# Kernel optimization log

Hardware: AMD Instinct MI355X
Metric: run time of the kernel (lower is better)

The kernel has to match this reference:

```python
import jax, jax.numpy as jnp
import numpy as np

P = 8  # patch_shape (8, 8) -> per-window sequence length 64


def _bias_indices():
    # pairs of (i, j) coords inside an 8x8 patch window
    pairs = np.array([[i, j] for i in range(P) for j in range(P)])  # [64, 2]
    rel = pairs[:, None, :] - pairs[None, :, :] + P - 1  # [64, 64, 2] in [0, 14]
    return rel[:, :, 0], rel[:, :, 1]


def _make_mask(Wy, Wx):
    # generate_mask with apply_shift=True, patch_shape=(8,8)
    s = P // 2
    m = np.zeros((Wy, Wx, P, P, P, P), dtype=bool)
    m[-1, :, :s, :, s:, :] = True
    m[-1, :, s:, :, :s, :] = True
    m[:, -1, :, :s, :, s:] = True
    m[:, -1, :, s:, :, :s] = True
    return jnp.asarray(m.reshape(Wy, Wx, P * P, P * P))


def setup_inputs() -> dict:
    key = jax.random.key(0)
    ks = jax.random.split(key, 10)
    B, Wy, Wx, S, E, H, hd = 16, 16, 16, 64, 128, 4, 32
    sc = 0.05
    return {
        "patches": jax.random.normal(ks[0], (B, Wy, Wx, S, E), dtype=jnp.float32),
        "Wq": jax.random.normal(ks[1], (H, E, hd), dtype=jnp.float32) * sc,
        "bq": jax.random.normal(ks[2], (H, hd), dtype=jnp.float32) * sc,
        "Wk": jax.random.normal(ks[3], (H, E, hd), dtype=jnp.float32) * sc,
        "bk": jax.random.normal(ks[4], (H, hd), dtype=jnp.float32) * sc,
        "Wv": jax.random.normal(ks[5], (H, E, hd), dtype=jnp.float32) * sc,
        "bv": jax.random.normal(ks[6], (H, hd), dtype=jnp.float32) * sc,
        "pos_bias": jax.random.normal(ks[7], (2 * P - 1, 2 * P - 1), dtype=jnp.float32) * 0.02,
        "Wo": jax.random.normal(ks[8], (E, E), dtype=jnp.float32) * sc,
        "bo": jax.random.normal(ks[9], (E,), dtype=jnp.float32) * sc,
        "mask": _make_mask(Wy, Wx),
    }


def reference(patches, Wq, bq, Wk, bk, Wv, bv, pos_bias, Wo, bo, mask):
    hd = Wq.shape[-1]
    B, Wy, Wx, S, E = patches.shape
    H = Wq.shape[0]
    # per-head Q/K/V projections (torch loops over heads; here batched over h)
    q = jnp.einsum("bvwse,hed->bvwhsd", patches, Wq) + bq[:, None, :]
    k = jnp.einsum("bvwse,hed->bvwhsd", patches, Wk) + bk[:, None, :]
    v = jnp.einsum("bvwse,hed->bvwhsd", patches, Wv) + bv[:, None, :]
    logits = jnp.einsum("bvwhqd,bvwhkd->bvwhqk", q, k) / jnp.sqrt(jnp.asarray(hd, patches.dtype))
    ri, ci = _bias_indices()
    logits = logits + pos_bias[ri, ci]  # gather [15,15] -> [64,64]
    logits = jnp.where(mask[None, :, :, None, :, :], -jnp.inf, logits)
    attn = jax.nn.softmax(logits, axis=-1)
    out = jnp.einsum("bvwhqk,bvwhkd->bvwhqd", attn, v)
    # concat heads: [..., H, S, hd] -> [..., S, H*hd]
    out = jnp.swapaxes(out, 3, 4).reshape(B, Wy, Wx, S, H * hd)
    return jnp.einsum("bvwse,ef->bvwsf", out, Wo) + bo
```

## Files before the change

kernel.cpp:

```cpp
#include <hip/hip_runtime.h>
#include <hip/hip_bf16.h>

typedef float f32x4 __attribute__((ext_vector_type(4)));
typedef short bf16x8 __attribute__((ext_vector_type(8)));
typedef short s16x4 __attribute__((ext_vector_type(4)));
typedef unsigned int u32;

#define MFMA16(a, b, c) __builtin_amdgcn_mfma_f32_16x16x32_bf16((a), (b), (c), 0, 0, 0)

__device__ __forceinline__ u32 pk2(float lo, float hi) {
    union { __hip_bfloat162 h; u32 u; } c;
    c.h = __float22bfloat162_rn(float2{lo, hi});
    return c.u;
}

__device__ __forceinline__ unsigned short f2bf(float x) {
    union { float f; unsigned int u; } a; a.f = x;
    unsigned int r = a.u + 0x7fffu + ((a.u >> 16) & 1u);
    return (unsigned short)(r >> 16);
}

__global__ void prep_kernel(const float* __restrict__ Wq, const float* __restrict__ bq,
                            const float* __restrict__ Wk, const float* __restrict__ bk,
                            const float* __restrict__ Wv, const float* __restrict__ bv,
                            const float* __restrict__ pos_bias, const float* __restrict__ Wo,
                            unsigned short* __restrict__ WT, unsigned short* __restrict__ WoT,
                            float* __restrict__ bqkv, float* __restrict__ bm) {
    const float LOG2E = 1.4426950408889634f;
    int t = blockIdx.x * blockDim.x + threadIdx.x;
    int nt = gridDim.x * blockDim.x;
    for (int i = t; i < 384 * 128; i += nt) {
        int c = i >> 7, kk = i & 127;
        int h = c / 96, rem = c - h * 96, p = rem >> 5, n = rem & 31;
        const float* W = (p == 0) ? Wq : (p == 1 ? Wk : Wv);
        WT[i] = f2bf(W[(h * 128 + kk) * 32 + n]);
    }
    for (int i = t; i < 128 * 128; i += nt) {
        int n = i >> 7, kk = i & 127;
        WoT[i] = f2bf(Wo[kk * 128 + n]);
    }
    for (int i = t; i < 384; i += nt) {
        int h = i / 96, rem = i - h * 96, p = rem >> 5, n = rem & 31;
        const float* b = (p == 0) ? bq : (p == 1 ? bk : bv);
        bqkv[i] = b[h * 32 + n];
    }
    for (int i = t; i < 4 * 4 * 4 * 64 * 4; i += nt) {
        int r = i & 3, l = (i >> 2) & 63, kt = (i >> 8) & 3, qt = (i >> 10) & 3, v = (i >> 12) & 3;
        int q = qt * 16 + (l & 15);
        int k = kt * 16 + ((l >> 4) << 2) + r;
        int qi = q >> 3, qj = q & 7, ki = k >> 3, kj = k & 7;
        bool masked = (((v >> 1) != 0) && ((qi < 4) != (ki < 4))) ||
                      (((v & 1) != 0) && ((qj < 4) != (kj < 4)));
        bm[i] = masked ? -1e30f : pos_bias[(qi - ki + 7) * 15 + (qj - kj + 7)] * LOG2E;
    }
}

__launch_bounds__(256, 3)
__global__ void swin_kernel(const float* __restrict__ patches,
                            const unsigned short* __restrict__ WT,
                            const float* __restrict__ bqkv,
                            const float* __restrict__ bm,
                            const unsigned short* __restrict__ WoT,
                            const float* __restrict__ bo,
                            float* __restrict__ out) {
    __shared__ short lds[16384];
    const int win = ((blockIdx.x & 7) << 9) | (blockIdx.x >> 3);
    const int tid = threadIdx.x;
    const int lane = tid & 63;
    const int h = tid >> 6;
    const int l15 = lane & 15, l4 = lane >> 4;
    const int sw15 = (l15 & 7) << 3;
    const f32x4 zero = {0.f, 0.f, 0.f, 0.f};
    const int sA = ((l4 & 1) << 5) + l15;
    const int sB = sA + 16;
    const float rs2 = 0.2550348660629988f;
    const float4* bmv = reinterpret_cast<const float4*>(bm);

    {
        const float4* src = reinterpret_cast<const float4*>(patches + (size_t)win * 8192);
        #pragma unroll
        for (int i = 0; i < 8; ++i) {
            int idx4 = i * 256 + tid;
            float4 v = src[idx4];
            int row = idx4 >> 5, col = (idx4 & 31) << 2;
            union { u32 u[2]; s16x4 s; } pk;
            pk.u[0] = pk2(v.x, v.y);
            pk.u[1] = pk2(v.z, v.w);
            *reinterpret_cast<s16x4*>(&lds[row * 128 + (col ^ ((row & 7) << 3))]) = pk.s;
        }
    }
    __syncthreads();

    bf16x8 xa[4][4];
    #pragma unroll
    for (int mt = 0; mt < 4; ++mt)
        #pragma unroll
        for (int ks = 0; ks < 4; ++ks)
            xa[mt][ks] = *reinterpret_cast<const bf16x8*>(
                &lds[(mt * 16 + l15) * 128 + ((ks * 32 + l4 * 8) ^ sw15)]);
    __syncthreads();

    bf16x8 qf[4], kf[4];
    #pragma unroll
    for (int ct = 0; ct < 4; ++ct) {
        bf16x8 wb[4];
        #pragma unroll
        for (int ks = 0; ks < 4; ++ks)
            wb[ks] = *reinterpret_cast<const bf16x8*>(
                &WT[(h * 96 + ct * 16 + l15) * 128 + ks * 32 + l4 * 8]);
        float b4[4];
        #pragma unroll
        for (int r = 0; r < 4; ++r) b4[r] = bqkv[h * 96 + ct * 16 + l4 * 4 + r];
        #pragma unroll
        for (int mt = 0; mt < 4; ++mt) {
            f32x4 a = zero;
            __builtin_amdgcn_s_setprio(1);
            #pragma unroll
            for (int ks = 0; ks < 4; ++ks) a = MFMA16(wb[ks], xa[mt][ks], a);
            __builtin_amdgcn_s_setprio(0);
            u32 pw0 = pk2(a[0] + b4[0], a[1] + b4[1]);
            u32 pw1 = pk2(a[2] + b4[2], a[3] + b4[3]);
            u32 e0 = __shfl(pw0, sA);
            u32 e1 = __shfl(pw1, sA);
            u32 e2 = __shfl(pw0, sB);
            u32 e3 = __shfl(pw1, sB);
            if ((ct & 1) == (l4 >> 1)) {
                union { u32 u[4]; bf16x8 v; } c;
                c.u[0] = e0; c.u[1] = e1; c.u[2] = e2; c.u[3] = e3;
                if (ct < 2) qf[mt] = c.v; else kf[mt] = c.v;
            }
        }
    }

    #pragma unroll
    for (int ctv = 0; ctv < 2; ++ctv) {
        bf16x8 wb[4];
        #pragma unroll
        for (int ks = 0; ks < 4; ++ks)
            wb[ks] = *reinterpret_cast<const bf16x8*>(
                &WT[(h * 96 + 64 + ctv * 16 + l15) * 128 + ks * 32 + l4 * 8]);
        float bb = bqkv[h * 96 + 64 + ctv * 16 + l15];
        __builtin_amdgcn_s_setprio(1);
        #pragma unroll
        for (int mt = 0; mt < 4; ++mt) {
            f32x4 a = zero;
            #pragma unroll
            for (int ks = 0; ks < 4; ++ks) a = MFMA16(xa[mt][ks], wb[ks], a);
            int n = ctv * 16 + l15;
            int tok0 = (mt * 16 + l4 * 4) ^ sw15;
            union { u32 u[2]; s16x4 s; } pk;
            pk.u[0] = pk2(a[0] + bb, a[1] + bb);
            pk.u[1] = pk2(a[2] + bb, a[3] + bb);
            *reinterpret_cast<s16x4*>(&lds[h * 2048 + n * 64 + tok0]) = pk.s;
        }
        __builtin_amdgcn_s_setprio(0);
    }

    bf16x8 vf[2][2];
    #pragma unroll
    for (int nt = 0; nt < 2; ++nt)
        #pragma unroll
        for (int ks = 0; ks < 2; ++ks)
            vf[nt][ks] = *reinterpret_cast<const bf16x8*>(
                &lds[h * 2048 + (nt * 16 + l15) * 64 + ((ks * 32 + l4 * 8) ^ sw15)]);

    f32x4 O[2][4];
    #pragma unroll
    for (int nt = 0; nt < 2; ++nt)
        #pragma unroll
        for (int qt = 0; qt < 4; ++qt) O[nt][qt] = zero;

    const int mv = (((win >> 4) & 15) == 15 ? 2 : 0) + ((win & 15) == 15 ? 1 : 0);

    float4 bcur[4], bnxt[4];
    #pragma unroll
    for (int kt = 0; kt < 4; ++kt) bcur[kt] = bmv[((mv * 4 + 0) * 4 + kt) * 64 + lane];

    #pragma unroll
    for (int qt = 0; qt < 4; ++qt) {
        f32x4 LT[4];
        __builtin_amdgcn_s_setprio(1);
        #pragma unroll
        for (int kt = 0; kt < 4; ++kt) LT[kt] = MFMA16(kf[kt], qf[qt], zero);
        __builtin_amdgcn_s_setprio(0);

        if (qt < 3) {
            #pragma unroll
            for (int kt = 0; kt < 4; ++kt)
                bnxt[kt] = bmv[((mv * 4 + qt + 1) * 4 + kt) * 64 + lane];
        }

        float x[4][4];
        float m = -3.0e38f;
        #pragma unroll
        for (int kt = 0; kt < 4; ++kt) {
            x[kt][0] = LT[kt][0] * rs2 + bcur[kt].x;
            x[kt][1] = LT[kt][1] * rs2 + bcur[kt].y;
            x[kt][2] = LT[kt][2] * rs2 + bcur[kt].z;
            x[kt][3] = LT[kt][3] * rs2 + bcur[kt].w;
            m = fmaxf(m, fmaxf(fmaxf(x[kt][0], x[kt][1]), fmaxf(x[kt][2], x[kt][3])));
        }
        m = fmaxf(m, __shfl_xor(m, 16));
        m = fmaxf(m, __shfl_xor(m, 32));
        float s = 0.f;
        #pragma unroll
        for (int kt = 0; kt < 4; ++kt)
            #pragma unroll
            for (int r = 0; r < 4; ++r) {
                float e = exp2f(x[kt][r] - m);
                x[kt][r] = e;
                s += e;
            }
        s += __shfl_xor(s, 16);
        s += __shfl_xor(s, 32);
        float inv = 1.0f / s;

        u32 wp[4][2];
        #pragma unroll
        for (int kt = 0; kt < 4; ++kt) {
            wp[kt][0] = pk2(x[kt][0] * inv, x[kt][1] * inv);
            wp[kt][1] = pk2(x[kt][2] * inv, x[kt][3] * inv);
        }
        u32 fr[2][4];
        #pragma unroll
        for (int kt = 0; kt < 4; ++kt) {
            u32 a0 = __shfl(wp[kt][0], sA);
            u32 a1 = __shfl(wp[kt][1], sA);
            u32 b0 = __shfl(wp[kt][0], sB);
            u32 b1 = __shfl(wp[kt][1], sB);
            if ((kt & 1) == (l4 >> 1)) {
                const int ks = kt >> 1;
                fr[ks][0] = a0; fr[ks][1] = a1; fr[ks][2] = b0; fr[ks][3] = b1;
            }
        }
        bf16x8 pf0, pf1;
        {
            union { u32 u[4]; bf16x8 v; } c0, c1;
            c0.u[0] = fr[0][0]; c0.u[1] = fr[0][1]; c0.u[2] = fr[0][2]; c0.u[3] = fr[0][3];
            c1.u[0] = fr[1][0]; c1.u[1] = fr[1][1]; c1.u[2] = fr[1][2]; c1.u[3] = fr[1][3];
            pf0 = c0.v; pf1 = c1.v;
        }
        __builtin_amdgcn_s_setprio(1);
        #pragma unroll
        for (int nt = 0; nt < 2; ++nt) {
            O[nt][qt] = MFMA16(vf[nt][0], pf0, O[nt][qt]);
            O[nt][qt] = MFMA16(vf[nt][1], pf1, O[nt][qt]);
        }
        __builtin_amdgcn_s_setprio(0);

        if (qt < 3) {
            #pragma unroll
            for (int kt = 0; kt < 4; ++kt) bcur[kt] = bnxt[kt];
        }
    }

    bf16x8 wf[2][4];
    #pragma unroll
    for (int nt = 0; nt < 2; ++nt)
        #pragma unroll
        for (int ks = 0; ks < 4; ++ks)
            wf[nt][ks] = *reinterpret_cast<const bf16x8*>(
                &WoT[(h * 32 + nt * 16 + l15) * 128 + ks * 32 + l4 * 8]);
    float4 bo4[2];
    #pragma unroll
    for (int nt = 0; nt < 2; ++nt)
        bo4[nt] = *reinterpret_cast<const float4*>(&bo[h * 32 + nt * 16 + l4 * 4]);

    #pragma unroll
    for (int nt = 0; nt < 2; ++nt)
        #pragma unroll
        for (int qt = 0; qt < 4; ++qt) {
            int q = qt * 16 + l15;
            int f0 = (h * 32 + nt * 16 + l4 * 4) ^ sw15;
            union { u32 u[2]; s16x4 s; } pk;
            pk.u[0] = pk2(O[nt][qt][0], O[nt][qt][1]);
            pk.u[1] = pk2(O[nt][qt][2], O[nt][qt][3]);
            *reinterpret_cast<s16x4*>(&lds[8192 + q * 128 + f0]) = pk.s;
        }
    __syncthreads();

    {
        float* outw = out + (size_t)win * 8192;
        #pragma unroll
        for (int mt = 0; mt < 4; ++mt) {
            bf16x8 af[4];
            #pragma unroll
            for (int ks = 0; ks < 4; ++ks)
                af[ks] = *reinterpret_cast<const bf16x8*>(
                    &lds[8192 + (mt * 16 + l15) * 128 + ((ks * 32 + l4 * 8) ^ sw15)]);
            __builtin_amdgcn_s_setprio(1);
            #pragma unroll
            for (int nt = 0; nt < 2; ++nt) {
                f32x4 a = zero;
                #pragma unroll
                for (int ks = 0; ks < 4; ++ks) a = MFMA16(wf[nt][ks], af[ks], a);
                float4 st;
                st.x = a[0] + bo4[nt].x;
                st.y = a[1] + bo4[nt].y;
                st.z = a[2] + bo4[nt].z;
                st.w = a[3] + bo4[nt].w;
                *reinterpret_cast<float4*>(
                    &outw[(size_t)(mt * 16 + l15) * 128 + h * 32 + nt * 16 + l4 * 4]) = st;
            }
            __builtin_amdgcn_s_setprio(0);
        }
    }
}

extern "C" void kernel_launch(void* const* d_in, const int* in_sizes, int n_in,
                              void* d_out, int out_size, void* d_ws, size_t ws_size,
                              hipStream_t stream) {
    const float* patches  = (const float*)d_in[0];
    const float* Wq       = (const float*)d_in[1];
    const float* bq       = (const float*)d_in[2];
    const float* Wk       = (const float*)d_in[3];
    const float* bk       = (const float*)d_in[4];
    const float* Wv       = (const float*)d_in[5];
    const float* bv       = (const float*)d_in[6];
    const float* pos_bias = (const float*)d_in[7];
    const float* Wo       = (const float*)d_in[8];
    const float* bo       = (const float*)d_in[9];

    char* ws = (char*)d_ws;
    unsigned short* WT  = (unsigned short*)(ws);
    unsigned short* WoT = (unsigned short*)(ws + 98304);
    float* bqkv         = (float*)(ws + 131072);
    float* bm           = (float*)(ws + 132608);

    hipLaunchKernelGGL(prep_kernel, dim3(64), dim3(256), 0, stream,
                       Wq, bq, Wk, bk, Wv, bv, pos_bias, Wo, WT, WoT, bqkv, bm);
    hipLaunchKernelGGL(swin_kernel, dim3(4096), dim3(256), 0, stream,
                       patches, WT, bqkv, bm, WoT, bo, (float*)d_out);
}
```

Before: 108.5 us.

## Process two windows per block and prefetch the second window's patches during compute

Each block now handles two consecutive windows, with half as many blocks launched. The second window's input is loaded into registers while the first window's projections and attention run, and its bf16 conversion into LDS overlaps the first window's output staging. The aim is to hide global load latency and amortize block setup. In exchange, each thread holds 8 extra float4 registers under a 3-waves bound, which risks spills or lower occupancy, and there are fewer blocks to spread across CUs.

```diff
diff --git a/kernel.cpp b/kernel.cpp
--- a/kernel.cpp
+++ b/kernel.cpp
@@ -55,52 +55,36 @@
     }
 }
 
-__launch_bounds__(256, 3)
-__global__ void swin_kernel(const float* __restrict__ patches,
-                            const unsigned short* __restrict__ WT,
-                            const float* __restrict__ bqkv,
-                            const float* __restrict__ bm,
-                            const unsigned short* __restrict__ WoT,
-                            const float* __restrict__ bo,
-                            float* __restrict__ out) {
-    __shared__ short lds[16384];
-    const int win = ((blockIdx.x & 7) << 9) | (blockIdx.x >> 3);
-    const int tid = threadIdx.x;
-    const int lane = tid & 63;
-    const int h = tid >> 6;
-    const int l15 = lane & 15, l4 = lane >> 4;
-    const int sw15 = (l15 & 7) << 3;
-    const f32x4 zero = {0.f, 0.f, 0.f, 0.f};
-    const int sA = ((l4 & 1) << 5) + l15;
-    const int sB = sA + 16;
-    const float rs2 = 0.2550348660629988f;
-    const float4* bmv = reinterpret_cast<const float4*>(bm);
-
-    {
-        const float4* src = reinterpret_cast<const float4*>(patches + (size_t)win * 8192);
-        #pragma unroll
-        for (int i = 0; i < 8; ++i) {
-            int idx4 = i * 256 + tid;
-            float4 v = src[idx4];
-            int row = idx4 >> 5, col = (idx4 & 31) << 2;
-            union { u32 u[2]; s16x4 s; } pk;
-            pk.u[0] = pk2(v.x, v.y);
-            pk.u[1] = pk2(v.z, v.w);
-            *reinterpret_cast<s16x4*>(&lds[row * 128 + (col ^ ((row & 7) << 3))]) = pk.s;
-        }
-    }
-    __syncthreads();
-
-    bf16x8 xa[4][4];
+
+__device__ __forceinline__ void cvt_to_xb(short* __restrict__ lds,
+                                          const float4 (&px)[8], int tid) {
+    #pragma unroll
+    for (int i = 0; i < 8; ++i) {
+        int idx4 = i * 256 + tid;
+        int row = idx4 >> 5, col = (idx4 & 31) << 2;
+        union { u32 u[2]; s16x4 s; } pk;
+        pk.u[0] = pk2(px[i].x, px[i].y);
+        pk.u[1] = pk2(px[i].z, px[i].w);
+        *reinterpret_cast<s16x4*>(&lds[row * 128 + (col ^ ((row & 7) << 3))]) = pk.s;
+    }
+}
+
+__device__ __forceinline__ void read_xa(const short* __restrict__ lds,
+                                        bf16x8 (&xa)[4][4], int l15, int l4, int sw15) {
     #pragma unroll
     for (int mt = 0; mt < 4; ++mt)
         #pragma unroll
         for (int ks = 0; ks < 4; ++ks)
             xa[mt][ks] = *reinterpret_cast<const bf16x8*>(
                 &lds[(mt * 16 + l15) * 128 + ((ks * 32 + l4 * 8) ^ sw15)]);
-    __syncthreads();
-
-    bf16x8 qf[4], kf[4];
+}
+
+__device__ __forceinline__ void proj_qk(const unsigned short* __restrict__ WT,
+                                        const float* __restrict__ bqkv,
+                                        const bf16x8 (&xa)[4][4],
+                                        bf16x8 (&qf)[4], bf16x8 (&kf)[4],
+                                        int h, int l15, int l4, int sA, int sB) {
+    const f32x4 zero = {0.f, 0.f, 0.f, 0.f};
     #pragma unroll
     for (int ct = 0; ct < 4; ++ct) {
         bf16x8 wb[4];
@@ -131,7 +115,14 @@
             }
         }
     }
-
+}
+
+__device__ __forceinline__ void proj_v(short* __restrict__ lds,
+                                       const unsigned short* __restrict__ WT,
+                                       const float* __restrict__ bqkv,
+                                       const bf16x8 (&xa)[4][4],
+                                       int h, int l15, int l4, int sw15) {
+    const f32x4 zero = {0.f, 0.f, 0.f, 0.f};
     #pragma unroll
     for (int ctv = 0; ctv < 2; ++ctv) {
         bf16x8 wb[4];
@@ -155,7 +146,16 @@
         }
         __builtin_amdgcn_s_setprio(0);
     }
-
+}
+
+__device__ __forceinline__ void attn_one(const short* __restrict__ lds,
+                                         const float4* __restrict__ bmv,
+                                         const bf16x8 (&qf)[4], const bf16x8 (&kf)[4],
+                                         f32x4 (&O)[2][4], int mv, int lane,
+                                         int h, int l15, int l4, int sw15,
+                                         int sA, int sB) {
+    const f32x4 zero = {0.f, 0.f, 0.f, 0.f};
+    const float rs2 = 0.2550348660629988f;
     bf16x8 vf[2][2];
     #pragma unroll
     for (int nt = 0; nt < 2; ++nt)
@@ -163,14 +163,10 @@
         for (int ks = 0; ks < 2; ++ks)
             vf[nt][ks] = *reinterpret_cast<const bf16x8*>(
                 &lds[h * 2048 + (nt * 16 + l15) * 64 + ((ks * 32 + l4 * 8) ^ sw15)]);
-
-    f32x4 O[2][4];
     #pragma unroll
     for (int nt = 0; nt < 2; ++nt)
         #pragma unroll
         for (int qt = 0; qt < 4; ++qt) O[nt][qt] = zero;
-
-    const int mv = (((win >> 4) & 15) == 15 ? 2 : 0) + ((win & 15) == 15 ? 1 : 0);
 
     float4 bcur[4], bnxt[4];
     #pragma unroll
@@ -253,19 +249,11 @@
             for (int kt = 0; kt < 4; ++kt) bcur[kt] = bnxt[kt];
         }
     }
-
-    bf16x8 wf[2][4];
-    #pragma unroll
-    for (int nt = 0; nt < 2; ++nt)
-        #pragma unroll
-        for (int ks = 0; ks < 4; ++ks)
-            wf[nt][ks] = *reinterpret_cast<const bf16x8*>(
-                &WoT[(h * 32 + nt * 16 + l15) * 128 + ks * 32 + l4 * 8]);
-    float4 bo4[2];
-    #pragma unroll
-    for (int nt = 0; nt < 2; ++nt)
-        bo4[nt] = *reinterpret_cast<const float4*>(&bo[h * 32 + nt * 16 + l4 * 4]);
-
+}
+
+__device__ __forceinline__ void write_attnout(short* __restrict__ lds,
+                                              const f32x4 (&O)[2][4],
+                                              int h, int l15, int l4, int sw15) {
     #pragma unroll
     for (int nt = 0; nt < 2; ++nt)
         #pragma unroll
@@ -277,34 +265,114 @@
             pk.u[1] = pk2(O[nt][qt][2], O[nt][qt][3]);
             *reinterpret_cast<s16x4*>(&lds[8192 + q * 128 + f0]) = pk.s;
         }
-    __syncthreads();
+}
+
+__device__ __forceinline__ void stage5_store(const short* __restrict__ lds,
+                                             const unsigned short* __restrict__ WoT,
+                                             const float* __restrict__ bo,
+                                             float* __restrict__ out, int win,
+                                             int h, int l15, int l4, int sw15) {
+    const f32x4 zero = {0.f, 0.f, 0.f, 0.f};
+    bf16x8 wf[2][4];
+    #pragma unroll
+    for (int nt = 0; nt < 2; ++nt)
+        #pragma unroll
+        for (int ks = 0; ks < 4; ++ks)
+            wf[nt][ks] = *reinterpret_cast<const bf16x8*>(
+                &WoT[(h * 32 + nt * 16 + l15) * 128 + ks * 32 + l4 * 8]);
+    float4 bo4[2];
+    #pragma unroll
+    for (int nt = 0; nt < 2; ++nt)
+        bo4[nt] = *reinterpret_cast<const float4*>(&bo[h * 32 + nt * 16 + l4 * 4]);
+    float* outw = out + (size_t)win * 8192;
+    #pragma unroll
+    for (int mt = 0; mt < 4; ++mt) {
+        bf16x8 af[4];
+        #pragma unroll
+        for (int ks = 0; ks < 4; ++ks)
+            af[ks] = *reinterpret_cast<const bf16x8*>(
+                &lds[8192 + (mt * 16 + l15) * 128 + ((ks * 32 + l4 * 8) ^ sw15)]);
+        __builtin_amdgcn_s_setprio(1);
+        #pragma unroll
+        for (int nt = 0; nt < 2; ++nt) {
+            f32x4 a = zero;
+            #pragma unroll
+            for (int ks = 0; ks < 4; ++ks) a = MFMA16(wf[nt][ks], af[ks], a);
+            float4 st;
+            st.x = a[0] + bo4[nt].x;
+            st.y = a[1] + bo4[nt].y;
+            st.z = a[2] + bo4[nt].z;
+            st.w = a[3] + bo4[nt].w;
+            *reinterpret_cast<float4*>(
+                &outw[(size_t)(mt * 16 + l15) * 128 + h * 32 + nt * 16 + l4 * 4]) = st;
+        }
+        __builtin_amdgcn_s_setprio(0);
+    }
+}
+
+__launch_bounds__(256, 3)
+__global__ void swin_kernel(const float* __restrict__ patches,
+                            const unsigned short* __restrict__ WT,
+                            const float* __restrict__ bqkv,
+                            const float* __restrict__ bm,
+                            const unsigned short* __restrict__ WoT,
+                            const float* __restrict__ bo,
+                            float* __restrict__ out) {
+    __shared__ short lds[16384];
+    const int swz = ((blockIdx.x & 7) << 8) | (blockIdx.x >> 3);
+    const int win0 = swz * 2, win1 = win0 + 1;
+    const int tid = threadIdx.x;
+    const int lane = tid & 63;
+    const int h = tid >> 6;
+    const int l15 = lane & 15, l4 = lane >> 4;
+    const int sw15 = (l15 & 7) << 3;
+    const int sA = ((l4 & 1) << 5) + l15;
+    const int sB = sA + 16;
+    const float4* bmv = reinterpret_cast<const float4*>(bm);
+    const int mv0 = (((win0 >> 4) & 15) == 15 ? 2 : 0) + ((win0 & 15) == 15 ? 1 : 0);
+    const int mv1 = (((win1 >> 4) & 15) == 15 ? 2 : 0) + ((win1 & 15) == 15 ? 1 : 0);
+
+    float4 px[8];
+    bf16x8 xa[4][4], qf[4], kf[4];
+    f32x4 O[2][4];
 
     {
-        float* outw = out + (size_t)win * 8192;
-        #pragma unroll
-        for (int mt = 0; mt < 4; ++mt) {
-            bf16x8 af[4];
-            #pragma unroll
-            for (int ks = 0; ks < 4; ++ks)
-                af[ks] = *reinterpret_cast<const bf16x8*>(
-                    &lds[8192 + (mt * 16 + l15) * 128 + ((ks * 32 + l4 * 8) ^ sw15)]);
-            __builtin_amdgcn_s_setprio(1);
-            #pragma unroll
-            for (int nt = 0; nt < 2; ++nt) {
-                f32x4 a = zero;
-                #pragma unroll
-                for (int ks = 0; ks < 4; ++ks) a = MFMA16(wf[nt][ks], af[ks], a);
-                float4 st;
-                st.x = a[0] + bo4[nt].x;
-                st.y = a[1] + bo4[nt].y;
-                st.z = a[2] + bo4[nt].z;
-                st.w = a[3] + bo4[nt].w;
-                *reinterpret_cast<float4*>(
-                    &outw[(size_t)(mt * 16 + l15) * 128 + h * 32 + nt * 16 + l4 * 4]) = st;
-            }
-            __builtin_amdgcn_s_setprio(0);
-        }
-    }
+        const float4* src = reinterpret_cast<const float4*>(patches + (size_t)win0 * 8192);
+        #pragma unroll
+        for (int i = 0; i < 8; ++i) px[i] = src[i * 256 + tid];
+    }
+    cvt_to_xb(lds, px, tid);
+    __syncthreads();
+
+    read_xa(lds, xa, l15, l4, sw15);
+    __syncthreads();
+
+    {
+        const float4* src = reinterpret_cast<const float4*>(patches + (size_t)win1 * 8192);
+        #pragma unroll
+        for (int i = 0; i < 8; ++i) px[i] = src[i * 256 + tid];
+    }
+
+    proj_qk(WT, bqkv, xa, qf, kf, h, l15, l4, sA, sB);
+    proj_v(lds, WT, bqkv, xa, h, l15, l4, sw15);
+    attn_one(lds, bmv, qf, kf, O, mv0, lane, h, l15, l4, sw15, sA, sB);
+    __syncthreads();
+
+    cvt_to_xb(lds, px, tid);
+    write_attnout(lds, O, h, l15, l4, sw15);
+    __syncthreads();
+
+    stage5_store(lds, WoT, bo, out, win0, h, l15, l4, sw15);
+    read_xa(lds, xa, l15, l4, sw15);
+    __syncthreads();
+
+    proj_qk(WT, bqkv, xa, qf, kf, h, l15, l4, sA, sB);
+    proj_v(lds, WT, bqkv, xa, h, l15, l4, sw15);
+    attn_one(lds, bmv, qf, kf, O, mv1, lane, h, l15, l4, sw15, sA, sB);
+    write_attnout(lds, O, h, l15, l4, sw15);
+    __syncthreads();
+
+    stage5_store(lds, WoT, bo, out, win1, h, l15, l4, sw15);
 }
 
 extern "C" void kernel_launch(void* const* d_in, const int* in_sizes, int n_in,
@@ -329,6 +397,6 @@
 
     hipLaunchKernelGGL(prep_kernel, dim3(64), dim3(256), 0, stream,
                        Wq, bq, Wk, bk, Wv, bv, pos_bias, Wo, WT, WoT, bqkv, bm);
-    hipLaunchKernelGGL(swin_kernel, dim3(4096), dim3(256), 0, stream,
+    hipLaunchKernelGGL(swin_kernel, dim3(2048), dim3(256), 0, stream,
                        patches, WT, bqkv, bm, WoT, bo, (float*)d_out);
 }
```

Result: slower. 159.2 us (+46.7%).
